# Optimization experiments

Measured on AMD Instinct MI355X. Metric: run time of the kernel, lower is better.

Reference implementation:

```python
import jax, jax.numpy as jnp
import numpy as np

THRESH = 0.5  # original code thresholds raw span logit channel 0 at 0.5


def setup_inputs() -> dict:
    key = jax.random.key(0)
    ks = jax.random.split(key, 9)
    B, S, H, P = 4, 256, 768, 54  # P = num_spo_patterns + 1
    scale = 0.02
    return {
        "sequence_output": jax.random.normal(ks[0], (B, S, H), jnp.float32),
        "W1s": jax.random.normal(ks[1], (H, H), jnp.float32) * scale,
        "b1s": jnp.zeros((H,), jnp.float32),
        "W2s": jax.random.normal(ks[2], (2, H), jnp.float32) * scale,
        "b2s": jnp.zeros((2,), jnp.float32),
        "Wp1": jax.random.normal(ks[3], (H, 2 * H), jnp.float32) * scale,
        "bp1": jnp.zeros((H,), jnp.float32),
        "Wp2": jax.random.normal(ks[4], (P, H), jnp.float32) * scale,
        "bp2": jnp.zeros((P,), jnp.float32),
    }


def reference(sequence_output, W1s, b1s, W2s, b2s, Wp1, bp1, Wp2, bp2):
    x = sequence_output                                # [B,S,H]
    B, S, H = x.shape
    # span classifier: Linear -> ReLU -> Linear
    h = jax.nn.relu(jnp.einsum('bsh,kh->bsk', x, W1s) + b1s)
    span_logits = jnp.einsum('bsh,kh->bsk', h, W2s) + b2s   # [B,S,2]
    cand = span_logits[..., 0] > THRESH                      # [B,S] candidates
    # spo pattern classifier on concat pairs: Linear(2H,H) splits into two H->H maps
    Wa, Wb = Wp1[:, :H], Wp1[:, H:]                          # subject / object halves
    ha = jnp.einsum('bsh,kh->bsk', x, Wa)                    # [B,S,H]
    hb = jnp.einsum('bsh,kh->bsk', x, Wb)                    # [B,S,H]
    pair_hidden = jax.nn.relu(ha[:, :, None, :] + hb[:, None, :, :] + bp1)  # [B,S,S,H]
    pair_logits = jnp.einsum('bijh,ph->bijp', pair_hidden, Wp2) + bp2       # [B,S,S,P]
    # valid pairs: both are candidates and subj != obj (diagonal excluded)
    not_diag = ~jnp.eye(S, dtype=bool)
    valid = cand[:, :, None] & cand[:, None, :] & not_diag   # [B,S,S]
    # dense masked equivalent of the per-pair Python loop (invalid pairs zeroed,
    # matching the zeros fallback for empty candidate sets)
    spo_pattern_logits = jnp.where(valid[..., None], pair_logits, 0.0)
    return spo_pattern_logits
```

## Files before the change

kernel.cpp:

```cpp
#include <hip/hip_runtime.h>
#include <hip/hip_bf16.h>


#define M_ROWS 1024
#define HDIM 768
#define PDIM 54
#define MAXC 256
#define KCHUNK 16
#define NKC (HDIM / KCHUNK)
#define KSPLIT 8
#define KSEG (HDIM / KSPLIT)

#define CANDCNT_OFF  0
#define PAIRCNT_OFF  4
#define CANDIDX_OFF  8192
#define CANDSLOT_OFF 12288
#define PAIR_OFF     16384
#define HPART_OFF    1064960

__global__ __launch_bounds__(256) void gemm_k_kernel(
    const float* __restrict__ x, const float* __restrict__ W1,
    float* __restrict__ hpart, int* __restrict__ counters)
{
    __shared__ float As[16][68];
    __shared__ float Bs[16][68];

    if (blockIdx.x == 0 && blockIdx.y == 0 && blockIdx.z == 0 && threadIdx.x < 2)
        counters[threadIdx.x] = 0;

    const int m0 = blockIdx.x * 64;
    const int n0 = blockIdx.y * 64;
    const int kb = blockIdx.z * KSEG;
    const int t  = threadIdx.x;
    const int tm = t & 15;
    const int tn = t >> 4;
    const int r  = t >> 2;
    const int c4 = (t & 3) * 4;

    float acc[4][4] = {};

    for (int k0 = kb; k0 < kb + KSEG; k0 += 16) {
        float4 av = *(const float4*)(x  + (size_t)(m0 + r) * HDIM + k0 + c4);
        float4 bv = *(const float4*)(W1 + (size_t)(n0 + r) * HDIM + k0 + c4);
        As[c4+0][r] = av.x; As[c4+1][r] = av.y; As[c4+2][r] = av.z; As[c4+3][r] = av.w;
        Bs[c4+0][r] = bv.x; Bs[c4+1][r] = bv.y; Bs[c4+2][r] = bv.z; Bs[c4+3][r] = bv.w;
        __syncthreads();
        #pragma unroll
        for (int kk = 0; kk < 16; ++kk) {
            float a[4], b[4];
            #pragma unroll
            for (int i = 0; i < 4; ++i) a[i] = As[kk][tm * 4 + i];
            #pragma unroll
            for (int j = 0; j < 4; ++j) b[j] = Bs[kk][tn * 4 + j];
            #pragma unroll
            for (int i = 0; i < 4; ++i)
                #pragma unroll
                for (int j = 0; j < 4; ++j)
                    acc[i][j] += a[i] * b[j];
        }
        __syncthreads();
    }

    float* dst = hpart + (size_t)blockIdx.z * (M_ROWS * HDIM);
    #pragma unroll
    for (int i = 0; i < 4; ++i) {
        float4 v = make_float4(acc[i][0], acc[i][1], acc[i][2], acc[i][3]);
        *(float4*)(dst + (size_t)(m0 + tm * 4 + i) * HDIM + n0 + tn * 4) = v;
    }
}

__global__ __launch_bounds__(256) void span_cand_kernel(
    const float* __restrict__ hpart, const float* __restrict__ b1,
    const float* __restrict__ w2row, const float* __restrict__ b2,
    int* __restrict__ candCount, int* __restrict__ candIdx,
    int* __restrict__ candSlot)
{
    const int m = blockIdx.x;
    const int t = threadIdx.x;
    float p = 0.f;
    for (int n = t; n < HDIM; n += 256) {
        float v = 0.f;
        #pragma unroll
        for (int z = 0; z < KSPLIT; ++z)
            v += hpart[(size_t)z * (M_ROWS * HDIM) + (size_t)m * HDIM + n];
        v += b1[n];
        v = v > 0.f ? v : 0.f;
        p += v * w2row[n];
    }
    __shared__ float wred[4];
    #pragma unroll
    for (int off = 32; off > 0; off >>= 1) p += __shfl_down(p, off, 64);
    if ((t & 63) == 0) wred[t >> 6] = p;
    __syncthreads();
    if (t == 0) {
        float s = wred[0] + wred[1] + wred[2] + wred[3] + b2[0];
        if (s > 0.5f) {
            int sl = atomicAdd(candCount, 1);
            if (sl < MAXC) { candIdx[sl] = m; candSlot[m] = sl; }
            else candSlot[m] = -1;
        } else {
            candSlot[m] = -1;
        }
    }
}

__global__ __launch_bounds__(256) void hab_kernel(
    const float* __restrict__ x, const float* __restrict__ Wp1,
    const int* __restrict__ candCount, const int* __restrict__ candIdx,
    float* __restrict__ ha, float* __restrict__ hb)
{
    __shared__ float xs[HDIM];
    __shared__ float red[2][KCHUNK][17];
    int nc = *candCount; if (nc > MAXC) nc = MAXC;
    const int nitems = nc * NKC;
    const int kk  = threadIdx.x >> 4;
    const int hb0 = (threadIdx.x & 15) * 4;

    for (int item = blockIdx.x; item < nitems; item += gridDim.x) {
        int slot = item / NKC;
        int kc   = item % NKC;
        int row  = candIdx[slot];

        for (int h = threadIdx.x; h < HDIM; h += 256)
            xs[h] = x[(size_t)row * HDIM + h];
        __syncthreads();

        int k = kc * KCHUNK + kk;
        const float* wr = Wp1 + (size_t)k * (2 * HDIM);
        float sa = 0.f, sb = 0.f;
        #pragma unroll
        for (int h = hb0; h < HDIM; h += 64) {
            float4 xv = *(const float4*)(xs + h);
            float4 wa = *(const float4*)(wr + h);
            float4 wb = *(const float4*)(wr + HDIM + h);
            sa += xv.x * wa.x + xv.y * wa.y + xv.z * wa.z + xv.w * wa.w;
            sb += xv.x * wb.x + xv.y * wb.y + xv.z * wb.z + xv.w * wb.w;
        }
        red[0][kk][threadIdx.x & 15] = sa;
        red[1][kk][threadIdx.x & 15] = sb;
        __syncthreads();

        if (threadIdx.x < 32) {
            int which = threadIdx.x >> 4;
            int kk2   = threadIdx.x & 15;
            float s = 0.f;
            #pragma unroll
            for (int g = 0; g < 16; ++g) s += red[which][kk2][g];
            float* dst = which == 0 ? ha : hb;
            dst[(size_t)slot * HDIM + kc * KCHUNK + kk2] = s;
        }
        __syncthreads();
    }
}

__global__ void pairs_kernel(const int* __restrict__ candSlot,
                             int* __restrict__ pairCount, int* __restrict__ pairList)
{
    int idx = blockIdx.x * 256 + threadIdx.x;
    int b = idx >> 16;
    int i = (idx >> 8) & 255;
    int j = idx & 255;
    if (i == j) return;
    if (candSlot[b * 256 + i] >= 0 && candSlot[b * 256 + j] >= 0) {
        int p = atomicAdd(pairCount, 1);
        pairList[p] = idx;
    }
}

__global__ __launch_bounds__(256) void pair_kernel(
    const float* __restrict__ ha, const float* __restrict__ hb,
    const float* __restrict__ bp1, const float* __restrict__ Wp2,
    const float* __restrict__ bp2, const int* __restrict__ candSlot,
    const int* __restrict__ pairCount, const int* __restrict__ pairList,
    float* __restrict__ out)
{
    __shared__ float v[HDIM];
    __shared__ float red[4][PDIM + 2];
    const int np = *pairCount;
    const int t = threadIdx.x;
    for (int p = blockIdx.x; p < np; p += gridDim.x) {
        int idx = pairList[p];
        int b = idx >> 16;
        int i = (idx >> 8) & 255;
        int j = idx & 255;
        int si = candSlot[b * 256 + i];
        int sj = candSlot[b * 256 + j];
        if (t < 192) {
            float4 a4 = *(const float4*)(ha + (size_t)si * HDIM + t * 4);
            float4 b4 = *(const float4*)(hb + (size_t)sj * HDIM + t * 4);
            float4 c4 = *(const float4*)(bp1 + t * 4);
            float4 r;
            r.x = a4.x + b4.x + c4.x; r.x = r.x > 0.f ? r.x : 0.f;
            r.y = a4.y + b4.y + c4.y; r.y = r.y > 0.f ? r.y : 0.f;
            r.z = a4.z + b4.z + c4.z; r.z = r.z > 0.f ? r.z : 0.f;
            r.w = a4.w + b4.w + c4.w; r.w = r.w > 0.f ? r.w : 0.f;
            *(float4*)(v + t * 4) = r;
        }
        __syncthreads();
        if (t < 216) {
            int pp  = t % PDIM;
            int seg = t / PDIM;
            const float* w = Wp2 + (size_t)pp * HDIM + seg * 192;
            const float* vv = v + seg * 192;
            float s = 0.f;
            for (int h = 0; h < 192; h += 4) {
                float4 a = *(const float4*)(vv + h);
                float4 b2_ = *(const float4*)(w + h);
                s += a.x * b2_.x + a.y * b2_.y + a.z * b2_.z + a.w * b2_.w;
            }
            red[seg][pp] = s;
        }
        __syncthreads();
        if (t < PDIM)
            out[(size_t)idx * PDIM + t] = red[0][t] + red[1][t] + red[2][t] + red[3][t] + bp2[t];
        __syncthreads();
    }
}

extern "C" void kernel_launch(void* const* d_in, const int* in_sizes, int n_in,
                              void* d_out, int out_size, void* d_ws, size_t ws_size,
                              hipStream_t stream) {
    const float* x   = (const float*)d_in[0];
    const float* W1s = (const float*)d_in[1];
    const float* b1s = (const float*)d_in[2];
    const float* W2s = (const float*)d_in[3];
    const float* b2s = (const float*)d_in[4];
    const float* Wp1 = (const float*)d_in[5];
    const float* bp1 = (const float*)d_in[6];
    const float* Wp2 = (const float*)d_in[7];
    const float* bp2 = (const float*)d_in[8];

    char* ws = (char*)d_ws;
    int*   counters = (int*)(ws + CANDCNT_OFF);
    int*   candCnt  = counters;
    int*   pairCnt  = counters + 1;
    int*   candIdx  = (int*)(ws + CANDIDX_OFF);
    int*   candSlot = (int*)(ws + CANDSLOT_OFF);
    int*   pairList = (int*)(ws + PAIR_OFF);
    float* hpart    = (float*)(ws + HPART_OFF);
    float* ha       = hpart + (size_t)KSPLIT * M_ROWS * HDIM;
    float* hb       = ha + (size_t)MAXC * HDIM;
    float* out = (float*)d_out;

    hipMemsetAsync(out, 0, (size_t)out_size * sizeof(float), stream);

    dim3 g(M_ROWS / 64, HDIM / 64, KSPLIT);
    gemm_k_kernel<<<g, 256, 0, stream>>>(x, W1s, hpart, counters);

    span_cand_kernel<<<M_ROWS, 256, 0, stream>>>(hpart, b1s, W2s, b2s,
                                                 candCnt, candIdx, candSlot);

    hab_kernel<<<2048, 256, 0, stream>>>(x, Wp1, candCnt, candIdx, ha, hb);

    pairs_kernel<<<1024, 256, 0, stream>>>(candSlot, pairCnt, pairList);

    pair_kernel<<<512, 256, 0, stream>>>(ha, hb, bp1, Wp2, bp2,
                                         candSlot, pairCnt, pairList, out);
}
```

Measured before the change: 140.6 us.

## Use split-bf16 MFMA GEMM with fused span epilogue for candidate scoring

Replaces the fp32 split-K SIMT GEMM and separate span reduction kernel with a convert pass that splits x and W1 into bf16 hi/lo pairs. An MFMA GEMM then uses three products to approximate fp32 accuracy and fuses bias, ReLU and the W2 dot product into its epilogue, accumulating span logits with atomics. This removes the large hpart write and read traffic and moves the matmul onto the matrix cores. It adds a conversion pass and uses atomics. The 3-term bf16 split may move logits near the 0.5 threshold, and atomic ordering makes the sums nondeterministic.

```diff
diff --git a/kernel.cpp b/kernel.cpp
--- a/kernel.cpp
+++ b/kernel.cpp
@@ -8,99 +8,129 @@
 #define MAXC 256
 #define KCHUNK 16
 #define NKC (HDIM / KCHUNK)
-#define KSPLIT 8
-#define KSEG (HDIM / KSPLIT)
-
-#define CANDCNT_OFF  0
-#define PAIRCNT_OFF  4
+
+#define CNT_OFF      0
+#define SPAN_OFF     4096
 #define CANDIDX_OFF  8192
 #define CANDSLOT_OFF 12288
 #define PAIR_OFF     16384
-#define HPART_OFF    1064960
-
-__global__ __launch_bounds__(256) void gemm_k_kernel(
+#define XH_OFF       1064960
+#define XL_OFF       2637824
+#define WH_OFF       4210688
+#define WL_OFF       5390336
+#define HA_OFF       6569984
+#define HB_OFF       7356416
+
+typedef short bf16x8 __attribute__((ext_vector_type(8)));
+typedef float f32x4  __attribute__((ext_vector_type(4)));
+
+__device__ __forceinline__ unsigned short f2bf(float f) {
+    unsigned u = __float_as_uint(f);
+    return (unsigned short)((u + 0x7FFFu + ((u >> 16) & 1u)) >> 16);
+}
+__device__ __forceinline__ float bf2f(unsigned short h) {
+    return __uint_as_float((unsigned)h << 16);
+}
+
+__global__ __launch_bounds__(256) void convert_kernel(
     const float* __restrict__ x, const float* __restrict__ W1,
-    float* __restrict__ hpart, int* __restrict__ counters)
-{
-    __shared__ float As[16][68];
-    __shared__ float Bs[16][68];
-
-    if (blockIdx.x == 0 && blockIdx.y == 0 && blockIdx.z == 0 && threadIdx.x < 2)
-        counters[threadIdx.x] = 0;
-
-    const int m0 = blockIdx.x * 64;
+    unsigned short* __restrict__ xh, unsigned short* __restrict__ xl,
+    unsigned short* __restrict__ wh, unsigned short* __restrict__ wl,
+    float* __restrict__ span, int* __restrict__ counters)
+{
+    int tid = blockIdx.x * 256 + threadIdx.x;
+    if (tid < 1024) span[tid] = 0.f;
+    if (tid < 2) counters[tid] = 0;
+
+    const int NX = (M_ROWS * HDIM) / 4;
+    float4 v;
+    unsigned short* dh; unsigned short* dl; int q;
+    if (tid < NX) {
+        v = ((const float4*)x)[tid];
+        dh = xh; dl = xl; q = tid;
+    } else {
+        q = tid - NX;
+        v = ((const float4*)W1)[q];
+        dh = wh; dl = wl;
+    }
+    ushort4 h, l;
+    h.x = f2bf(v.x); l.x = f2bf(v.x - bf2f(h.x));
+    h.y = f2bf(v.y); l.y = f2bf(v.y - bf2f(h.y));
+    h.z = f2bf(v.z); l.z = f2bf(v.z - bf2f(h.z));
+    h.w = f2bf(v.w); l.w = f2bf(v.w - bf2f(h.w));
+    ((ushort4*)dh)[q] = h;
+    ((ushort4*)dl)[q] = l;
+}
+
+__global__ __launch_bounds__(256) void gemm_span_mfma(
+    const unsigned short* __restrict__ xh, const unsigned short* __restrict__ xl,
+    const unsigned short* __restrict__ wh, const unsigned short* __restrict__ wl,
+    const float* __restrict__ b1, const float* __restrict__ w2row,
+    float* __restrict__ span)
+{
+    const int t = threadIdx.x;
+    const int wave = t >> 6, lane = t & 63;
+    const int quad = lane >> 4, c = lane & 15;
+    const int m0 = blockIdx.x * 64 + wave * 16;
     const int n0 = blockIdx.y * 64;
-    const int kb = blockIdx.z * KSEG;
-    const int t  = threadIdx.x;
-    const int tm = t & 15;
-    const int tn = t >> 4;
-    const int r  = t >> 2;
-    const int c4 = (t & 3) * 4;
-
-    float acc[4][4] = {};
-
-    for (int k0 = kb; k0 < kb + KSEG; k0 += 16) {
-        float4 av = *(const float4*)(x  + (size_t)(m0 + r) * HDIM + k0 + c4);
-        float4 bv = *(const float4*)(W1 + (size_t)(n0 + r) * HDIM + k0 + c4);
-        As[c4+0][r] = av.x; As[c4+1][r] = av.y; As[c4+2][r] = av.z; As[c4+3][r] = av.w;
-        Bs[c4+0][r] = bv.x; Bs[c4+1][r] = bv.y; Bs[c4+2][r] = bv.z; Bs[c4+3][r] = bv.w;
-        __syncthreads();
-        #pragma unroll
-        for (int kk = 0; kk < 16; ++kk) {
-            float a[4], b[4];
-            #pragma unroll
-            for (int i = 0; i < 4; ++i) a[i] = As[kk][tm * 4 + i];
-            #pragma unroll
-            for (int j = 0; j < 4; ++j) b[j] = Bs[kk][tn * 4 + j];
-            #pragma unroll
-            for (int i = 0; i < 4; ++i)
-                #pragma unroll
-                for (int j = 0; j < 4; ++j)
-                    acc[i][j] += a[i] * b[j];
-        }
-        __syncthreads();
-    }
-
-    float* dst = hpart + (size_t)blockIdx.z * (M_ROWS * HDIM);
+
+    const unsigned short* xhp = xh + (size_t)(m0 + c) * HDIM + quad * 8;
+    const unsigned short* xlp = xl + (size_t)(m0 + c) * HDIM + quad * 8;
+    const unsigned short* whp = wh + (size_t)(n0 + c) * HDIM + quad * 8;
+    const unsigned short* wlp = wl + (size_t)(n0 + c) * HDIM + quad * 8;
+
+    f32x4 acc[4] = {};
+
+    #pragma unroll 2
+    for (int k0 = 0; k0 < HDIM; k0 += 32) {
+        bf16x8 Ah = *(const bf16x8*)(xhp + k0);
+        bf16x8 Al = *(const bf16x8*)(xlp + k0);
+        #pragma unroll
+        for (int nt = 0; nt < 4; ++nt) {
+            bf16x8 Bh = *(const bf16x8*)(whp + (size_t)nt * 16 * HDIM + k0);
+            bf16x8 Bl = *(const bf16x8*)(wlp + (size_t)nt * 16 * HDIM + k0);
+            acc[nt] = __builtin_amdgcn_mfma_f32_16x16x32_bf16(Ah, Bh, acc[nt], 0, 0, 0);
+            acc[nt] = __builtin_amdgcn_mfma_f32_16x16x32_bf16(Ah, Bl, acc[nt], 0, 0, 0);
+            acc[nt] = __builtin_amdgcn_mfma_f32_16x16x32_bf16(Al, Bh, acc[nt], 0, 0, 0);
+        }
+    }
+
+    float part[4] = {0.f, 0.f, 0.f, 0.f};
     #pragma unroll
-    for (int i = 0; i < 4; ++i) {
-        float4 v = make_float4(acc[i][0], acc[i][1], acc[i][2], acc[i][3]);
-        *(float4*)(dst + (size_t)(m0 + tm * 4 + i) * HDIM + n0 + tn * 4) = v;
-    }
-}
-
-__global__ __launch_bounds__(256) void span_cand_kernel(
-    const float* __restrict__ hpart, const float* __restrict__ b1,
-    const float* __restrict__ w2row, const float* __restrict__ b2,
-    int* __restrict__ candCount, int* __restrict__ candIdx,
-    int* __restrict__ candSlot)
-{
-    const int m = blockIdx.x;
-    const int t = threadIdx.x;
-    float p = 0.f;
-    for (int n = t; n < HDIM; n += 256) {
-        float v = 0.f;
-        #pragma unroll
-        for (int z = 0; z < KSPLIT; ++z)
-            v += hpart[(size_t)z * (M_ROWS * HDIM) + (size_t)m * HDIM + n];
-        v += b1[n];
-        v = v > 0.f ? v : 0.f;
-        p += v * w2row[n];
-    }
-    __shared__ float wred[4];
+    for (int nt = 0; nt < 4; ++nt) {
+        int n_abs = n0 + nt * 16 + c;
+        float b1v = b1[n_abs], w2v = w2row[n_abs];
+        #pragma unroll
+        for (int r = 0; r < 4; ++r) {
+            float h = acc[nt][r] + b1v;
+            h = h > 0.f ? h : 0.f;
+            part[r] += h * w2v;
+        }
+    }
     #pragma unroll
-    for (int off = 32; off > 0; off >>= 1) p += __shfl_down(p, off, 64);
-    if ((t & 63) == 0) wred[t >> 6] = p;
-    __syncthreads();
-    if (t == 0) {
-        float s = wred[0] + wred[1] + wred[2] + wred[3] + b2[0];
-        if (s > 0.5f) {
-            int sl = atomicAdd(candCount, 1);
-            if (sl < MAXC) { candIdx[sl] = m; candSlot[m] = sl; }
-            else candSlot[m] = -1;
-        } else {
-            candSlot[m] = -1;
-        }
+    for (int mask = 1; mask < 16; mask <<= 1) {
+        #pragma unroll
+        for (int r = 0; r < 4; ++r) part[r] += __shfl_xor(part[r], mask, 64);
+    }
+    if (c < 4) {
+        #pragma unroll
+        for (int r = 0; r < 4; ++r)
+            if (c == r) atomicAdd(&span[m0 + quad * 4 + r], part[r]);
+    }
+}
+
+__global__ void cand_kernel(const float* __restrict__ span, const float* __restrict__ b2,
+                            int* __restrict__ candCount, int* __restrict__ candIdx,
+                            int* __restrict__ candSlot)
+{
+    int i = blockIdx.x * 256 + threadIdx.x;
+    float v = span[i] + b2[0];
+    if (v > 0.5f) {
+        int s = atomicAdd(candCount, 1);
+        if (s < MAXC) { candIdx[s] = i; candSlot[i] = s; }
+        else candSlot[i] = -1;
+    } else {
+        candSlot[i] = -1;
     }
 }
 
@@ -231,24 +261,29 @@
     const float* bp2 = (const float*)d_in[8];
 
     char* ws = (char*)d_ws;
-    int*   counters = (int*)(ws + CANDCNT_OFF);
+    int*   counters = (int*)(ws + CNT_OFF);
     int*   candCnt  = counters;
     int*   pairCnt  = counters + 1;
+    float* span     = (float*)(ws + SPAN_OFF);
     int*   candIdx  = (int*)(ws + CANDIDX_OFF);
     int*   candSlot = (int*)(ws + CANDSLOT_OFF);
     int*   pairList = (int*)(ws + PAIR_OFF);
-    float* hpart    = (float*)(ws + HPART_OFF);
-    float* ha       = hpart + (size_t)KSPLIT * M_ROWS * HDIM;
-    float* hb       = ha + (size_t)MAXC * HDIM;
+    unsigned short* xh = (unsigned short*)(ws + XH_OFF);
+    unsigned short* xl = (unsigned short*)(ws + XL_OFF);
+    unsigned short* wh = (unsigned short*)(ws + WH_OFF);
+    unsigned short* wl = (unsigned short*)(ws + WL_OFF);
+    float* ha       = (float*)(ws + HA_OFF);
+    float* hb       = (float*)(ws + HB_OFF);
     float* out = (float*)d_out;
 
     hipMemsetAsync(out, 0, (size_t)out_size * sizeof(float), stream);
 
-    dim3 g(M_ROWS / 64, HDIM / 64, KSPLIT);
-    gemm_k_kernel<<<g, 256, 0, stream>>>(x, W1s, hpart, counters);
-
-    span_cand_kernel<<<M_ROWS, 256, 0, stream>>>(hpart, b1s, W2s, b2s,
-                                                 candCnt, candIdx, candSlot);
+    convert_kernel<<<1344, 256, 0, stream>>>(x, W1s, xh, xl, wh, wl, span, counters);
+
+    dim3 gg(M_ROWS / 64, HDIM / 64);
+    gemm_span_mfma<<<gg, 256, 0, stream>>>(xh, xl, wh, wl, b1s, W2s, span);
+
+    cand_kernel<<<4, 256, 0, stream>>>(span, b2s, candCnt, candIdx, candSlot);
 
     hab_kernel<<<2048, 256, 0, stream>>>(x, Wp1, candCnt, candIdx, ha, hb);
 
```

Result: slower. 153.5 us (+9.2%).
